# Performance work log

Hardware: AMD Instinct MI355X
Metric: run time of the kernel (lower is better)

The kernel has to match this reference:

```python
import jax, jax.numpy as jnp
import numpy as np

B, T, F = 2048, 96, 32
H = 1024
G_EMB = 16
LSTM_IN = F + 11 + 1 + G_EMB  # 60


def _lstm_cell(x, h, c, W_ih, W_hh, b):
    g = x @ W_ih.T + h @ W_hh.T + b
    i, f, gg, o = jnp.split(g, 4, axis=-1)  # torch gate order: i, f, g, o
    c_new = jax.nn.sigmoid(f) * c + jax.nn.sigmoid(i) * jnp.tanh(gg)
    h_new = jax.nn.sigmoid(o) * jnp.tanh(c_new)
    return h_new, c_new


def setup_inputs() -> dict:
    key = jax.random.key(0)
    ks = jax.random.split(key, 26)
    s = 1.0 / np.sqrt(H)
    inp = {
        "dec_known": jax.random.normal(ks[0], (B, T, F), jnp.float32),
        "target_y": jax.random.normal(ks[1], (B, T, 1), jnp.float32),
        "enc_h": jax.random.normal(ks[2], (2, B, H), jnp.float32),
        "enc_c": jax.random.normal(ks[3], (2, B, H), jnp.float32),
        "last_enc_consumption": jax.random.normal(ks[4], (B, 1), jnp.float32),
        "group_ids": jax.random.randint(ks[5], (B,), 0, 1000),
        "cat_province": jax.random.randint(ks[6], (B,), 0, 13),
        "cat_customer_type": jax.random.randint(ks[7], (B,), 0, 2),
        "cat_price_type": jax.random.randint(ks[8], (B,), 0, 5),
        "cat_consumption_level": jax.random.randint(ks[9], (B,), 0, 3),
        # learned parameters
        "group_emb": jax.random.normal(ks[10], (1000, G_EMB), jnp.float32),
        "emb_province": jax.random.normal(ks[11], (13, 4), jnp.float32),
        "emb_customer_type": jax.random.normal(ks[12], (2, 2), jnp.float32),
        "emb_price_type": jax.random.normal(ks[13], (5, 3), jnp.float32),
        "emb_consumption_level": jax.random.normal(ks[14], (3, 2), jnp.float32),
        "W_ih0": jax.random.normal(ks[15], (4 * H, LSTM_IN), jnp.float32) * s,
        "W_hh0": jax.random.normal(ks[16], (4 * H, H), jnp.float32) * s,
        "b0": jax.random.normal(ks[17], (4 * H,), jnp.float32) * s,
        "W_ih1": jax.random.normal(ks[18], (4 * H, H), jnp.float32) * s,
        "W_hh1": jax.random.normal(ks[19], (4 * H, H), jnp.float32) * s,
        "b1": jax.random.normal(ks[20], (4 * H,), jnp.float32) * s,
        "W_proj": jax.random.normal(ks[21], (1, H), jnp.float32) * s,
        "b_proj": jnp.zeros((1,), jnp.float32),
    }
    return inp


def reference(dec_known, target_y, enc_h, enc_c, last_enc_consumption,
              group_ids, cat_province, cat_customer_type, cat_price_type,
              cat_consumption_level, group_emb, emb_province, emb_customer_type,
              emb_price_type, emb_consumption_level, W_ih0, W_hh0, b0,
              W_ih1, W_hh1, b1, W_proj, b_proj):
    b, t, _ = dec_known.shape
    # static per-sample features (categorical + group embeddings)
    cat_emb = jnp.concatenate([
        emb_province[cat_province], emb_customer_type[cat_customer_type],
        emb_price_type[cat_price_type], emb_consumption_level[cat_consumption_level],
    ], axis=-1)  # [B, 11]
    group_vec = group_emb[group_ids]  # [B, 16]
    static = jnp.concatenate([cat_emb, group_vec], axis=-1)  # [B, 27]
    # teacher_forcing_ratio = 1.0 => prev_y is last_enc_consumption then target_y shifted
    prev_y = jnp.concatenate([last_enc_consumption[:, None, :], target_y[:, :-1, :]], axis=1)  # [B,T,1]
    x = jnp.concatenate([
        prev_y, dec_known,
        jnp.broadcast_to(static[:, None, :], (b, t, static.shape[-1])),
    ], axis=-1)  # [B, T, 60]

    def step(carry, x_t):
        h1, c1, h2, c2 = carry
        h1, c1 = _lstm_cell(x_t, h1, c1, W_ih0, W_hh0, b0)
        h2, c2 = _lstm_cell(h1, h2, c2, W_ih1, W_hh1, b1)
        return (h1, c1, h2, c2), h2

    init = (enc_h[0], enc_c[0], enc_h[1], enc_c[1])
    _, hs = jax.lax.scan(step, init, jnp.swapaxes(x, 0, 1))  # hs: [T, B, H]
    y = jnp.einsum('tbh,oh->bto', hs, W_proj) + b_proj  # [B, T, 1]
    return y
```

## Files before the change

### kernel.cpp

```cpp
#include <hip/hip_runtime.h>
#include <hip/hip_bf16.h>
#include <stdint.h>


#define BB  2048
#define TT  96
#define NG  4096
#define NT0 34
#define NT1 64

typedef __bf16 bf16;
typedef __bf16 bf16x8 __attribute__((ext_vector_type(8)));
typedef float  f32x4  __attribute__((ext_vector_type(4)));

__device__ __forceinline__ float sigm(float x) { return 1.0f / (1.0f + __expf(-x)); }
__device__ __forceinline__ float ftanh(float x) { return 2.0f / (1.0f + __expf(-2.0f * x)) - 1.0f; }

__device__ __forceinline__ void gload16(const bf16* g, bf16* l) {
  __builtin_amdgcn_global_load_lds((const __attribute__((address_space(1))) void*)g,
                                   (__attribute__((address_space(3))) void*)l, 16, 0, 0);
}

#define SB()  __builtin_amdgcn_sched_barrier(0)
#define BAR() __builtin_amdgcn_s_barrier()


__global__ __launch_bounds__(256) void build_wf1(const float* __restrict__ Wih1,
                                                 const float* __restrict__ Whh1,
                                                 bf16* __restrict__ Wf) {
  int idx = blockIdx.x * 256 + threadIdx.x;
  if (idx >= 16 * NT1 * 8192) return;
  int j = idx & 7, lane = (idx >> 3) & 63, gf = (idx >> 9) & 7;
  int wg = (idx >> 12) & 1, kt = (idx >> 13) & 63, panel = idx >> 19;
  int np = panel * 256 + wg * 128 + gf * 16 + (lane & 15);
  int k  = kt * 32 + ((lane >> 4) << 3) + j;
  int n  = (np & 3) * 1024 + (np >> 2);
  float v = (k < 1024) ? Wih1[n * 1024 + k] : Whh1[n * 1024 + (k - 1024)];
  Wf[idx] = (bf16)v;
}

__global__ __launch_bounds__(256) void build_wf0(const float* __restrict__ Wih0,
                                                 const float* __restrict__ Whh0,
                                                 bf16* __restrict__ Wf) {
  int idx = blockIdx.x * 256 + threadIdx.x;
  if (idx >= 16 * NT0 * 8192) return;
  int j = idx & 7, lane = (idx >> 3) & 63, gf = (idx >> 9) & 7;
  int wg = (idx >> 12) & 1;
  int rem = idx >> 13;
  int kt = rem % NT0, panel = rem / NT0;
  int np = panel * 256 + wg * 128 + gf * 16 + (lane & 15);
  int k  = kt * 32 + ((lane >> 4) << 3) + j;
  int n  = (np & 3) * 1024 + (np >> 2);
  float v;
  if (k < 60)      v = Wih0[n * 60 + k];
  else if (k < 64) v = 0.0f;
  else             v = Whh0[n * 1024 + (k - 64)];
  Wf[idx] = (bf16)v;
}

__global__ __launch_bounds__(256) void perm_bias(const float* __restrict__ b0,
                                                 const float* __restrict__ b1,
                                                 float* __restrict__ b0p,
                                                 float* __restrict__ b1p) {
  int idx = blockIdx.x * 256 + threadIdx.x;
  if (idx >= NG) return;
  int n = (idx & 3) * 1024 + (idx >> 2);
  b0p[idx] = b0[n];
  b1p[idx] = b1[n];
}

__global__ __launch_bounds__(256) void build_x(
    const float* __restrict__ dec, const float* __restrict__ ty, const float* __restrict__ lec,
    const int* __restrict__ gid, const int* __restrict__ cp, const int* __restrict__ cct,
    const int* __restrict__ cpt, const int* __restrict__ ccl,
    const float* __restrict__ gemb, const float* __restrict__ ep, const float* __restrict__ ect,
    const float* __restrict__ ept, const float* __restrict__ ecl,
    bf16* __restrict__ X) {
  int idx = blockIdx.x * 256 + threadIdx.x;
  if (idx >= BB * TT) return;
  int b = idx / TT, t = idx % TT;
  bf16* x = X + (size_t)idx * 64;
  x[0] = (bf16)((t == 0) ? lec[b] : ty[b * TT + t - 1]);
  const float* d = dec + (size_t)idx * 32;
  #pragma unroll
  for (int k = 0; k < 32; ++k) x[1 + k] = (bf16)d[k];
  const float* e;
  e = ep  + cp[b]  * 4;  for (int j = 0; j < 4;  ++j) x[33 + j] = (bf16)e[j];
  e = ect + cct[b] * 2;  for (int j = 0; j < 2;  ++j) x[37 + j] = (bf16)e[j];
  e = ept + cpt[b] * 3;  for (int j = 0; j < 3;  ++j) x[39 + j] = (bf16)e[j];
  e = ecl + ccl[b] * 2;  for (int j = 0; j < 2;  ++j) x[42 + j] = (bf16)e[j];
  e = gemb + gid[b] * 16; for (int j = 0; j < 16; ++j) x[44 + j] = (bf16)e[j];
  for (int j = 60; j < 64; ++j) x[j] = (bf16)0.0f;
}

__global__ __launch_bounds__(256) void init_state(const float* __restrict__ enc_h,
                                                  const float* __restrict__ enc_c,
                                                  bf16* __restrict__ H1b,
                                                  bf16* __restrict__ H2b,
                                                  float* __restrict__ c1t,
                                                  float* __restrict__ c2t) {
  int idx = blockIdx.x * 256 + threadIdx.x;
  if (idx >= BB * 1024) return;
  int b = idx >> 10, h = idx & 1023;
  H1b[idx] = (bf16)enc_h[idx];
  H2b[idx] = (bf16)enc_h[(size_t)BB * 1024 + idx];
  c1t[(size_t)h * BB + b] = enc_c[idx];
  c2t[(size_t)h * BB + b] = enc_c[(size_t)BB * 1024 + idx];
}


template <int MODE>
__device__ __forceinline__ void body(
    int tm, int tn, int t,
    const bf16* __restrict__ P0, const bf16* __restrict__ P1,
    const bf16* __restrict__ Wf, const float* __restrict__ bperm,
    float* __restrict__ ct, bf16* __restrict__ Hout,
    const float* __restrict__ wp, const float* __restrict__ bp,
    float* __restrict__ y, bf16* As)
{
  constexpr int NT = MODE ? NT1 : NT0;

  const int tid = threadIdx.x;
  const int lane = tid & 63, w = tid >> 6;
  const int lrow = lane & 15, u = lane >> 4;
  const int wb = w & 1, wg = w >> 1;

  f32x4 acc[8][4];
  #pragma unroll
  for (int gf = 0; gf < 8; ++gf)
    #pragma unroll
    for (int bf = 0; bf < 4; ++bf) acc[gf][bf] = (f32x4){0.f, 0.f, 0.f, 0.f};

  const int r0 = tid >> 2, r1 = (256 + tid) >> 2;
  const int kc0 = (((tid & 3) ^ ((r0 >> 1) & 3)) << 3);
  const int kc1 = (((tid & 3) ^ ((r1 >> 1) & 3)) << 3);
  const int d0 = (tid & ~63) * 8;
  const int d1 = 2048 + d0;
  const int klocal = ((((lane >> 4) ^ (lrow >> 1)) & 3) << 3);

  auto aptr = [&](int row, int kt, int kc) -> const bf16* {
    if constexpr (MODE == 0) {
      return (kt < 2) ? (P0 + ((size_t)(tm + row) * TT + t) * 64 + kt * 32 + kc)
                      : (P1 + (size_t)(tm + row) * 1024 + (kt - 2) * 32 + kc);
    } else {
      return (kt < 32) ? (P0 + (size_t)(tm + row) * 1024 + kt * 32 + kc)
                       : (P1 + (size_t)(tm + row) * 1024 + (kt - 32) * 32 + kc);
    }
  };
  auto stageA = [&](int kt, bf16* buf) {
    gload16(aptr(r0, kt, kc0), buf + d0);
    gload16(aptr(r1, kt, kc1), buf + d1);
  };

  const bf16* wfbase = Wf + (size_t)(tn >> 8) * NT * 8192 + wg * 4096 + lane * 8;
  auto loadW = [&](bf16x8 (&wf)[8], int kt) {
    const bf16* p = wfbase + (size_t)kt * 8192;
    #pragma unroll
    for (int gf = 0; gf < 8; ++gf)
      wf[gf] = *reinterpret_cast<const bf16x8*>(p + gf * 512);
  };

  bf16x8 wfA[8], wfB[8];

  stageA(0, As);
  loadW(wfA, 0);
  stageA(1, As + 4096);
  asm volatile("s_waitcnt vmcnt(10)" ::: "memory");
  SB(); BAR(); SB();

  auto iter = [&](int kt, bf16x8 (&cur)[8], bf16x8 (&nxt)[8]) {
    bf16* buf = As + ((kt & 1) ? 4096 : 0);
    bf16x8 af[4];
    #pragma unroll
    for (int bf = 0; bf < 4; ++bf)
      af[bf] = *reinterpret_cast<const bf16x8*>(&buf[(wb * 64 + bf * 16 + lrow) * 32 + klocal]);
    asm volatile("s_waitcnt lgkmcnt(0)" ::: "memory");
    SB(); BAR(); SB();
    if (kt + 2 < NT) stageA(kt + 2, buf);
    if (kt + 1 < NT) loadW(nxt, kt + 1);
    SB();
    __builtin_amdgcn_s_setprio(1);
    #pragma unroll
    for (int gf = 0; gf < 8; ++gf)
      #pragma unroll
      for (int bf = 0; bf < 4; ++bf)
        acc[gf][bf] = __builtin_amdgcn_mfma_f32_16x16x32_bf16(cur[gf], af[bf], acc[gf][bf], 0, 0, 0);
    __builtin_amdgcn_s_setprio(0);
    if (kt + 2 < NT)      { asm volatile("s_waitcnt vmcnt(10)" ::: "memory"); }
    else if (kt + 1 < NT) { asm volatile("s_waitcnt vmcnt(8)" ::: "memory"); }
    else                  { asm volatile("s_waitcnt vmcnt(0)" ::: "memory"); }
    SB(); BAR(); SB();
  };

  for (int kt = 0; kt < NT; kt += 2) {
    iter(kt,     wfA, wfB);
    iter(kt + 1, wfB, wfA);
  }

  bf16* hst = As + w * 2048;
  const int hq = (tn >> 2) + wg * 32;
  const int bgb = tm + wb * 64;
  float yp[4] = {0.f, 0.f, 0.f, 0.f};

  #pragma unroll
  for (int gf = 0; gf < 8; ++gf) {
    int hg = hq + gf * 4 + u;
    f32x4 bv = *reinterpret_cast<const f32x4*>(&bperm[hg * 4]);
    float wph = 0.f;
    if constexpr (MODE == 1) wph = wp[hg];
    #pragma unroll
    for (int bf = 0; bf < 4; ++bf) {
      int bg = bgb + bf * 16 + lrow;
      float gi = acc[gf][bf][0] + bv[0];
      float gf_ = acc[gf][bf][1] + bv[1];
      float gg = acc[gf][bf][2] + bv[2];
      float go = acc[gf][bf][3] + bv[3];
      float* cp_ = ct + (size_t)hg * BB + bg;
      float c = *cp_;
      float cn = sigm(gf_) * c + sigm(gi) * ftanh(gg);
      float hn = sigm(go) * ftanh(cn);
      *cp_ = cn;
      hst[(bf * 16 + lrow) * 32 + gf * 4 + u] = (bf16)hn;
      if constexpr (MODE == 1) yp[bf] += hn * wph;
    }
  }

  asm volatile("s_waitcnt lgkmcnt(0)" ::: "memory");
  SB();

  #pragma unroll
  for (int q = 0; q < 4; ++q) {
    int chunk = q * 64 + lane;
    int row = chunk >> 2, seg = chunk & 3;
    bf16x8 v = *reinterpret_cast<const bf16x8*>(&hst[row * 32 + seg * 8]);
    *reinterpret_cast<bf16x8*>(&Hout[(size_t)(bgb + row) * 1024 + hq + seg * 8]) = v;
  }

  if constexpr (MODE == 1) {
    #pragma unroll
    for (int bf = 0; bf < 4; ++bf) {
      float s = yp[bf];
      s += __shfl_xor(s, 16);
      s += __shfl_xor(s, 32);
      if (lane < 16)
        atomicAdd(&y[(size_t)(bgb + bf * 16 + lane) * TT + t], s);
    }
  } else {
    if (tn == 0 && tid < 128) y[(size_t)(tm + tid) * TT + t] = bp[0];
  }
}

__global__ __launch_bounds__(256, 2) void step_kernel(
    const bf16* __restrict__ H1in, const bf16* __restrict__ H2in,
    bf16* __restrict__ H1out, bf16* __restrict__ H2out,
    const bf16* __restrict__ X,
    const bf16* __restrict__ Wf0, const bf16* __restrict__ Wf1,
    const float* __restrict__ b0p, const float* __restrict__ b1p,
    float* __restrict__ c1t, float* __restrict__ c2t,
    const float* __restrict__ wp, const float* __restrict__ bp,
    float* __restrict__ y, int t2, int only_l1) {
  __shared__ alignas(16) bf16 As[2 * 4096];
  int bid = (int)blockIdx.x;
  if (only_l1 || bid >= 256) {
    int v = only_l1 ? bid : bid - 256;
    int t1 = t2 + 1;
    if (t1 >= TT) return;
    int x = v & 7, r = v >> 3;
    int tm = (r & 15) << 7;
    int tn = ((x << 1) + (r >> 4)) << 8;
    body<0>(tm, tn, t1, X, H1in, Wf0, b0p, c1t, H1out, nullptr, bp, y, As);
  } else {
    int x = bid & 7, r = bid >> 3;
    int tm = (r & 15) << 7;
    int tn = ((x << 1) + (r >> 4)) << 8;
    body<1>(tm, tn, t2, H1in, H2in, Wf1, b1p, c2t, H2out, wp, nullptr, y, As);
  }
}


extern "C" void kernel_launch(void* const* d_in, const int* in_sizes, int n_in,
                              void* d_out, int out_size, void* d_ws, size_t ws_size,
                              hipStream_t stream) {
  const float* dec   = (const float*)d_in[0];
  const float* ty    = (const float*)d_in[1];
  const float* enc_h = (const float*)d_in[2];
  const float* enc_c = (const float*)d_in[3];
  const float* lec   = (const float*)d_in[4];
  const int*   gid   = (const int*)d_in[5];
  const int*   cp    = (const int*)d_in[6];
  const int*   cct   = (const int*)d_in[7];
  const int*   cpt   = (const int*)d_in[8];
  const int*   ccl   = (const int*)d_in[9];
  const float* gemb  = (const float*)d_in[10];
  const float* ep    = (const float*)d_in[11];
  const float* ect   = (const float*)d_in[12];
  const float* ept   = (const float*)d_in[13];
  const float* ecl   = (const float*)d_in[14];
  const float* Wih0  = (const float*)d_in[15];
  const float* Whh0  = (const float*)d_in[16];
  const float* b0    = (const float*)d_in[17];
  const float* Wih1  = (const float*)d_in[18];
  const float* Whh1  = (const float*)d_in[19];
  const float* b1    = (const float*)d_in[20];
  const float* wp    = (const float*)d_in[21];
  const float* bp    = (const float*)d_in[22];
  float* y = (float*)d_out;

  char* ws = (char*)d_ws;
  bf16* Wf1   = (bf16*)ws;  ws += (size_t)16 * NT1 * 8192 * 2;
  bf16* Wf0   = (bf16*)ws;  ws += (size_t)16 * NT0 * 8192 * 2;
  bf16* X     = (bf16*)ws;  ws += (size_t)BB * TT * 64 * 2;
  bf16* H1a   = (bf16*)ws;  ws += (size_t)BB * 1024 * 2;
  bf16* H1b   = (bf16*)ws;  ws += (size_t)BB * 1024 * 2;
  bf16* H2a   = (bf16*)ws;  ws += (size_t)BB * 1024 * 2;
  bf16* H2b   = (bf16*)ws;  ws += (size_t)BB * 1024 * 2;
  float* c1t  = (float*)ws; ws += (size_t)BB * 1024 * 4;
  float* c2t  = (float*)ws; ws += (size_t)BB * 1024 * 4;
  float* b0p  = (float*)ws; ws += (size_t)NG * 4;
  float* b1p  = (float*)ws; ws += (size_t)NG * 4;

  build_wf1<<<(16 * NT1 * 8192) / 256, 256, 0, stream>>>(Wih1, Whh1, Wf1);
  build_wf0<<<(16 * NT0 * 8192 + 255) / 256, 256, 0, stream>>>(Wih0, Whh0, Wf0);
  perm_bias<<<NG / 256, 256, 0, stream>>>(b0, b1, b0p, b1p);
  build_x<<<(BB * TT + 255) / 256, 256, 0, stream>>>(dec, ty, lec, gid, cp, cct, cpt, ccl,
                                                     gemb, ep, ect, ept, ecl, X);
  init_state<<<(BB * 1024) / 256, 256, 0, stream>>>(enc_h, enc_c, H1b, H2b, c1t, c2t);

  step_kernel<<<256, 256, 0, stream>>>(H1b, nullptr, H1a, nullptr, X, Wf0, Wf1,
                                       b0p, b1p, c1t, c2t, wp, bp, y, -1, 1);
  for (int t = 0; t < TT; ++t) {
    bf16* h1i = (t & 1) ? H1b : H1a;
    bf16* h1o = (t & 1) ? H1a : H1b;
    bf16* h2i = (t & 1) ? H2a : H2b;
    bf16* h2o = (t & 1) ? H2b : H2a;
    step_kernel<<<512, 256, 0, stream>>>(h1i, h2i, h1o, h2o, X, Wf0, Wf1,
                                         b0p, b1p, c1t, c2t, wp, bp, y, t, 0);
  }
}
```

Before: 6.392 ms.

## Store activations in MFMA fragment layout and load A directly to registers

```diff
diff --git a/kernel.cpp b/kernel.cpp
--- a/kernel.cpp
+++ b/kernel.cpp
@@ -16,13 +16,7 @@
 __device__ __forceinline__ float sigm(float x) { return 1.0f / (1.0f + __expf(-x)); }
 __device__ __forceinline__ float ftanh(float x) { return 2.0f / (1.0f + __expf(-2.0f * x)) - 1.0f; }
 
-__device__ __forceinline__ void gload16(const bf16* g, bf16* l) {
-  __builtin_amdgcn_global_load_lds((const __attribute__((address_space(1))) void*)g,
-                                   (__attribute__((address_space(3))) void*)l, 16, 0, 0);
-}
-
-#define SB()  __builtin_amdgcn_sched_barrier(0)
-#define BAR() __builtin_amdgcn_s_barrier()
+#define SB() __builtin_amdgcn_sched_barrier(0)
 
 
 __global__ __launch_bounds__(256) void build_wf1(const float* __restrict__ Wih1,
@@ -69,28 +63,33 @@
   b1p[idx] = b1[n];
 }
 
-__global__ __launch_bounds__(256) void build_x(
+__global__ __launch_bounds__(256) void build_xf(
     const float* __restrict__ dec, const float* __restrict__ ty, const float* __restrict__ lec,
     const int* __restrict__ gid, const int* __restrict__ cp, const int* __restrict__ cct,
     const int* __restrict__ cpt, const int* __restrict__ ccl,
     const float* __restrict__ gemb, const float* __restrict__ ep, const float* __restrict__ ect,
     const float* __restrict__ ept, const float* __restrict__ ecl,
-    bf16* __restrict__ X) {
+    bf16* __restrict__ Xf) {
   int idx = blockIdx.x * 256 + threadIdx.x;
   if (idx >= BB * TT) return;
   int b = idx / TT, t = idx % TT;
-  bf16* x = X + (size_t)idx * 64;
-  x[0] = (bf16)((t == 0) ? lec[b] : ty[b * TT + t - 1]);
+  float xv[64];
+  xv[0] = (t == 0) ? lec[b] : ty[b * TT + t - 1];
   const float* d = dec + (size_t)idx * 32;
   #pragma unroll
-  for (int k = 0; k < 32; ++k) x[1 + k] = (bf16)d[k];
+  for (int k = 0; k < 32; ++k) xv[1 + k] = d[k];
   const float* e;
-  e = ep  + cp[b]  * 4;  for (int j = 0; j < 4;  ++j) x[33 + j] = (bf16)e[j];
-  e = ect + cct[b] * 2;  for (int j = 0; j < 2;  ++j) x[37 + j] = (bf16)e[j];
-  e = ept + cpt[b] * 3;  for (int j = 0; j < 3;  ++j) x[39 + j] = (bf16)e[j];
-  e = ecl + ccl[b] * 2;  for (int j = 0; j < 2;  ++j) x[42 + j] = (bf16)e[j];
-  e = gemb + gid[b] * 16; for (int j = 0; j < 16; ++j) x[44 + j] = (bf16)e[j];
-  for (int j = 60; j < 64; ++j) x[j] = (bf16)0.0f;
+  e = ep  + cp[b]  * 4;  for (int j = 0; j < 4;  ++j) xv[33 + j] = e[j];
+  e = ect + cct[b] * 2;  for (int j = 0; j < 2;  ++j) xv[37 + j] = e[j];
+  e = ept + cpt[b] * 3;  for (int j = 0; j < 3;  ++j) xv[39 + j] = e[j];
+  e = ecl + ccl[b] * 2;  for (int j = 0; j < 2;  ++j) xv[42 + j] = e[j];
+  e = gemb + gid[b] * 16; for (int j = 0; j < 16; ++j) xv[44 + j] = e[j];
+  for (int j = 60; j < 64; ++j) xv[j] = 0.0f;
+  bf16* slab = Xf + (size_t)t * BB * 64;
+  int bt = b >> 4, bl = b & 15;
+  #pragma unroll
+  for (int k = 0; k < 64; ++k)
+    slab[((size_t)(bt * 8 + (k >> 3)) << 7) + bl * 8 + (k & 7)] = (bf16)xv[k];
 }
 
 __global__ __launch_bounds__(256) void init_state(const float* __restrict__ enc_h,
@@ -102,8 +101,9 @@
   int idx = blockIdx.x * 256 + threadIdx.x;
   if (idx >= BB * 1024) return;
   int b = idx >> 10, h = idx & 1023;
-  H1b[idx] = (bf16)enc_h[idx];
-  H2b[idx] = (bf16)enc_h[(size_t)BB * 1024 + idx];
+  size_t off = ((size_t)((b >> 4) * 128 + (h >> 3)) << 7) + ((b & 15) << 3) + (h & 7);
+  H1b[off] = (bf16)enc_h[idx];
+  H2b[off] = (bf16)enc_h[(size_t)BB * 1024 + idx];
   c1t[(size_t)h * BB + b] = enc_c[idx];
   c2t[(size_t)h * BB + b] = enc_c[(size_t)BB * 1024 + idx];
 }
@@ -116,7 +116,7 @@
     const bf16* __restrict__ Wf, const float* __restrict__ bperm,
     float* __restrict__ ct, bf16* __restrict__ Hout,
     const float* __restrict__ wp, const float* __restrict__ bp,
-    float* __restrict__ y, bf16* As)
+    float* __restrict__ y, bf16* hst_all)
 {
   constexpr int NT = MODE ? NT1 : NT0;
 
@@ -131,25 +131,22 @@
     #pragma unroll
     for (int bf = 0; bf < 4; ++bf) acc[gf][bf] = (f32x4){0.f, 0.f, 0.f, 0.f};
 
-  const int r0 = tid >> 2, r1 = (256 + tid) >> 2;
-  const int kc0 = (((tid & 3) ^ ((r0 >> 1) & 3)) << 3);
-  const int kc1 = (((tid & 3) ^ ((r1 >> 1) & 3)) << 3);
-  const int d0 = (tid & ~63) * 8;
-  const int d1 = 2048 + d0;
-  const int klocal = ((((lane >> 4) ^ (lrow >> 1)) & 3) << 3);
-
-  auto aptr = [&](int row, int kt, int kc) -> const bf16* {
-    if constexpr (MODE == 0) {
-      return (kt < 2) ? (P0 + ((size_t)(tm + row) * TT + t) * 64 + kt * 32 + kc)
-                      : (P1 + (size_t)(tm + row) * 1024 + (kt - 2) * 32 + kc);
-    } else {
-      return (kt < 32) ? (P0 + (size_t)(tm + row) * 1024 + kt * 32 + kc)
-                       : (P1 + (size_t)(tm + row) * 1024 + (kt - 32) * 32 + kc);
+  const int aoff = (u << 7) + (lrow << 3);
+  const int BtB = (tm >> 4) + wb * 4;
+
+  auto loadA = [&](bf16x8 (&af)[4], int kt) {
+    #pragma unroll
+    for (int bf = 0; bf < 4; ++bf) {
+      const bf16* p;
+      if constexpr (MODE == 0) {
+        p = (kt < 2) ? P0 + ((size_t)((BtB + bf) * 8 + kt * 4) << 7) + aoff
+                     : P1 + ((size_t)((BtB + bf) * 128 + (kt - 2) * 4) << 7) + aoff;
+      } else {
+        p = (kt < 32) ? P0 + ((size_t)((BtB + bf) * 128 + kt * 4) << 7) + aoff
+                      : P1 + ((size_t)((BtB + bf) * 128 + (kt - 32) * 4) << 7) + aoff;
+      }
+      af[bf] = *reinterpret_cast<const bf16x8*>(p);
     }
-  };
-  auto stageA = [&](int kt, bf16* buf) {
-    gload16(aptr(r0, kt, kc0), buf + d0);
-    gload16(aptr(r1, kt, kc1), buf + d1);
   };
 
   const bf16* wfbase = Wf + (size_t)(tn >> 8) * NT * 8192 + wg * 4096 + lane * 8;
@@ -160,44 +157,31 @@
       wf[gf] = *reinterpret_cast<const bf16x8*>(p + gf * 512);
   };
 
-  bf16x8 wfA[8], wfB[8];
-
-  stageA(0, As);
-  loadW(wfA, 0);
-  stageA(1, As + 4096);
-  asm volatile("s_waitcnt vmcnt(10)" ::: "memory");
-  SB(); BAR(); SB();
-
-  auto iter = [&](int kt, bf16x8 (&cur)[8], bf16x8 (&nxt)[8]) {
-    bf16* buf = As + ((kt & 1) ? 4096 : 0);
-    bf16x8 af[4];
-    #pragma unroll
-    for (int bf = 0; bf < 4; ++bf)
-      af[bf] = *reinterpret_cast<const bf16x8*>(&buf[(wb * 64 + bf * 16 + lrow) * 32 + klocal]);
-    asm volatile("s_waitcnt lgkmcnt(0)" ::: "memory");
-    SB(); BAR(); SB();
-    if (kt + 2 < NT) stageA(kt + 2, buf);
-    if (kt + 1 < NT) loadW(nxt, kt + 1);
+  bf16x8 afA[4], afB[4], wfA[8], wfB[8];
+
+  loadA(afA, 0); loadW(wfA, 0);
+  for (int kt = 0; kt < NT; kt += 2) {
+    if (kt + 1 < NT) { loadA(afB, kt + 1); loadW(wfB, kt + 1); }
     SB();
     __builtin_amdgcn_s_setprio(1);
     #pragma unroll
     for (int gf = 0; gf < 8; ++gf)
       #pragma unroll
       for (int bf = 0; bf < 4; ++bf)
-        acc[gf][bf] = __builtin_amdgcn_mfma_f32_16x16x32_bf16(cur[gf], af[bf], acc[gf][bf], 0, 0, 0);
+        acc[gf][bf] = __builtin_amdgcn_mfma_f32_16x16x32_bf16(wfA[gf], afA[bf], acc[gf][bf], 0, 0, 0);
     __builtin_amdgcn_s_setprio(0);
-    if (kt + 2 < NT)      { asm volatile("s_waitcnt vmcnt(10)" ::: "memory"); }
-    else if (kt + 1 < NT) { asm volatile("s_waitcnt vmcnt(8)" ::: "memory"); }
-    else                  { asm volatile("s_waitcnt vmcnt(0)" ::: "memory"); }
-    SB(); BAR(); SB();
-  };
-
-  for (int kt = 0; kt < NT; kt += 2) {
-    iter(kt,     wfA, wfB);
-    iter(kt + 1, wfB, wfA);
-  }
-
-  bf16* hst = As + w * 2048;
+    if (kt + 2 < NT) { loadA(afA, kt + 2); loadW(wfA, kt + 2); }
+    SB();
+    __builtin_amdgcn_s_setprio(1);
+    #pragma unroll
+    for (int gf = 0; gf < 8; ++gf)
+      #pragma unroll
+      for (int bf = 0; bf < 4; ++bf)
+        acc[gf][bf] = __builtin_amdgcn_mfma_f32_16x16x32_bf16(wfB[gf], afB[bf], acc[gf][bf], 0, 0, 0);
+    __builtin_amdgcn_s_setprio(0);
+  }
+
+  bf16* hst = hst_all + w * 2048;
   const int hq = (tn >> 2) + wg * 32;
   const int bgb = tm + wb * 64;
   float yp[4] = {0.f, 0.f, 0.f, 0.f};
@@ -233,7 +217,9 @@
     int chunk = q * 64 + lane;
     int row = chunk >> 2, seg = chunk & 3;
     bf16x8 v = *reinterpret_cast<const bf16x8*>(&hst[row * 32 + seg * 8]);
-    *reinterpret_cast<bf16x8*>(&Hout[(size_t)(bgb + row) * 1024 + hq + seg * 8]) = v;
+    size_t off = ((size_t)(((bgb >> 4) + (row >> 4)) * 128 + (hq >> 3) + seg) << 7)
+               + ((row & 15) << 3);
+    *reinterpret_cast<bf16x8*>(&Hout[off]) = v;
   }
 
   if constexpr (MODE == 1) {
@@ -253,13 +239,13 @@
 __global__ __launch_bounds__(256, 2) void step_kernel(
     const bf16* __restrict__ H1in, const bf16* __restrict__ H2in,
     bf16* __restrict__ H1out, bf16* __restrict__ H2out,
-    const bf16* __restrict__ X,
+    const bf16* __restrict__ Xf,
     const bf16* __restrict__ Wf0, const bf16* __restrict__ Wf1,
     const float* __restrict__ b0p, const float* __restrict__ b1p,
     float* __restrict__ c1t, float* __restrict__ c2t,
     const float* __restrict__ wp, const float* __restrict__ bp,
     float* __restrict__ y, int t2, int only_l1) {
-  __shared__ alignas(16) bf16 As[2 * 4096];
+  __shared__ alignas(16) bf16 hst_all[4 * 2048];
   int bid = (int)blockIdx.x;
   if (only_l1 || bid >= 256) {
     int v = only_l1 ? bid : bid - 256;
@@ -268,12 +254,14 @@
     int x = v & 7, r = v >> 3;
     int tm = (r & 15) << 7;
     int tn = ((x << 1) + (r >> 4)) << 8;
-    body<0>(tm, tn, t1, X, H1in, Wf0, b0p, c1t, H1out, nullptr, bp, y, As);
+    body<0>(tm, tn, t1, Xf + (size_t)t1 * BB * 64, H1in,
+            Wf0, b0p, c1t, H1out, nullptr, bp, y, hst_all);
   } else {
     int x = bid & 7, r = bid >> 3;
     int tm = (r & 15) << 7;
     int tn = ((x << 1) + (r >> 4)) << 8;
-    body<1>(tm, tn, t2, H1in, H2in, Wf1, b1p, c2t, H2out, wp, nullptr, y, As);
+    body<1>(tm, tn, t2, H1in, H2in,
+            Wf1, b1p, c2t, H2out, wp, nullptr, y, hst_all);
   }
 }
 
@@ -309,7 +297,7 @@
   char* ws = (char*)d_ws;
   bf16* Wf1   = (bf16*)ws;  ws += (size_t)16 * NT1 * 8192 * 2;
   bf16* Wf0   = (bf16*)ws;  ws += (size_t)16 * NT0 * 8192 * 2;
-  bf16* X     = (bf16*)ws;  ws += (size_t)BB * TT * 64 * 2;
+  bf16* Xf    = (bf16*)ws;  ws += (size_t)BB * TT * 64 * 2;
   bf16* H1a   = (bf16*)ws;  ws += (size_t)BB * 1024 * 2;
   bf16* H1b   = (bf16*)ws;  ws += (size_t)BB * 1024 * 2;
   bf16* H2a   = (bf16*)ws;  ws += (size_t)BB * 1024 * 2;
@@ -322,18 +310,18 @@
   build_wf1<<<(16 * NT1 * 8192) / 256, 256, 0, stream>>>(Wih1, Whh1, Wf1);
   build_wf0<<<(16 * NT0 * 8192 + 255) / 256, 256, 0, stream>>>(Wih0, Whh0, Wf0);
   perm_bias<<<NG / 256, 256, 0, stream>>>(b0, b1, b0p, b1p);
-  build_x<<<(BB * TT + 255) / 256, 256, 0, stream>>>(dec, ty, lec, gid, cp, cct, cpt, ccl,
-                                                     gemb, ep, ect, ept, ecl, X);
+  build_xf<<<(BB * TT + 255) / 256, 256, 0, stream>>>(dec, ty, lec, gid, cp, cct, cpt, ccl,
+                                                      gemb, ep, ect, ept, ecl, Xf);
   init_state<<<(BB * 1024) / 256, 256, 0, stream>>>(enc_h, enc_c, H1b, H2b, c1t, c2t);
 
-  step_kernel<<<256, 256, 0, stream>>>(H1b, nullptr, H1a, nullptr, X, Wf0, Wf1,
+  step_kernel<<<256, 256, 0, stream>>>(H1b, nullptr, H1a, nullptr, Xf, Wf0, Wf1,
                                        b0p, b1p, c1t, c2t, wp, bp, y, -1, 1);
   for (int t = 0; t < TT; ++t) {
     bf16* h1i = (t & 1) ? H1b : H1a;
     bf16* h1o = (t & 1) ? H1a : H1b;
     bf16* h2i = (t & 1) ? H2a : H2b;
     bf16* h2o = (t & 1) ? H2b : H2a;
-    step_kernel<<<512, 256, 0, stream>>>(h1i, h2i, h1o, h2o, X, Wf0, Wf1,
+    step_kernel<<<512, 256, 0, stream>>>(h1i, h2i, h1o, h2o, Xf, Wf0, Wf1,
                                          b0p, b1p, c1t, c2t, wp, bp, y, t, 0);
   }
 }
```

New measurement: 5.921 ms. 7.4% less time.
